# Kernel tuning notes

Measured on AMD Instinct MI355X. Metric: run time of the kernel, lower is better.

## Reference

```python
import jax, jax.numpy as jnp
import numpy as np

N_CAT, N_PER = 5, 20
N_NODES = N_CAT * N_PER  # 100
T, IN_DIM, H = 512, 256, 1024


def gru_seq(x, Wih, Whh, bih, bhh):
    # x: (B, T, IN). torch GRU (batch_first), returns all hidden states (B, T, H).
    B = x.shape[0]
    Hd = Whh.shape[1]
    xp = x @ Wih.T + bih  # (B, T, 3H) precomputed input projections

    def step(h, xt):
        gh = h @ Whh.T + bhh
        xr, xz, xn = jnp.split(xt, 3, axis=-1)
        hr, hz, hn = jnp.split(gh, 3, axis=-1)
        r = jax.nn.sigmoid(xr + hr)
        z = jax.nn.sigmoid(xz + hz)
        n = jnp.tanh(xn + r * hn)
        h_new = (1.0 - z) * n + z * h
        return h_new, h_new

    h0 = jnp.zeros((B, Hd), x.dtype)
    _, hs = jax.lax.scan(step, h0, jnp.swapaxes(xp, 0, 1))
    return jnp.swapaxes(hs, 0, 1)  # (B, T, H)


def attention_block(x, Wt, bt):
    # x: (B, T, D). Linear over the time axis, softmax over output-time axis.
    # w[b,u,d] = sum_t x[b,t,d] * Wt[u,t] + bt[u]
    w = jnp.einsum('btd,ut->bud', x, Wt) + bt[None, :, None]
    probs = jax.nn.softmax(w, axis=1)  # softmax over u (time) per (b, d)
    return jnp.sum(probs * x, axis=1)  # (B, D)


def gat_conv(x, edge_index, W, a_src, a_dst, bias):
    # Single-head PyG GATConv with default add_self_loops=True, neg slope 0.2.
    N = x.shape[0]
    loops = jnp.arange(N)
    src = jnp.concatenate([edge_index[0], loops])
    dst = jnp.concatenate([edge_index[1], loops])
    h = x @ W.T  # (N, D)
    alpha_s = h @ a_src  # (N,)
    alpha_d = h @ a_dst
    e = jax.nn.leaky_relu(alpha_s[src] + alpha_d[dst], negative_slope=0.2)
    # segment softmax over incoming edges per target node
    emax = jax.ops.segment_max(e, dst, num_segments=N)
    ex = jnp.exp(e - emax[dst])
    denom = jax.ops.segment_sum(ex, dst, num_segments=N)
    alpha = ex / denom[dst]
    out = jax.ops.segment_sum(alpha[:, None] * h[src], dst, num_segments=N)
    return out + bias


def setup_inputs() -> dict:
    key = jax.random.key(0)
    ks = jax.random.split(key, 24)
    s = 0.05

    def rn(k, shape):
        return jax.random.normal(k, shape, dtype=jnp.float32) * s

    # structured edge lists
    inner = []
    for c in range(N_CAT):
        for i in range(N_PER):
            for j in range(N_PER):
                if i != j:
                    inner.append((c * N_PER + i, c * N_PER + j))
    inner_edge = jnp.asarray(np.array(inner, dtype=np.int64).T)  # (2, 1900)
    outer = [(i, j) for i in range(N_CAT) for j in range(N_CAT) if i != j]
    outer_edge = jnp.asarray(np.array(outer, dtype=np.int64).T)  # (2, 20)

    return {
        'weekly_batch': jax.random.normal(ks[0], (N_NODES, T, IN_DIM), dtype=jnp.float32),
        'gru_Wih': rn(ks[1], (3 * H, IN_DIM)),
        'gru_Whh': rn(ks[2], (3 * H, H)),
        'gru_bih': rn(ks[3], (3 * H,)),
        'gru_bhh': rn(ks[4], (3 * H,)),
        'enc_att_W': rn(ks[5], (T, T)),
        'enc_att_b': rn(ks[6], (T,)),
        'pool_att_W': rn(ks[7], (N_PER, N_PER)),
        'pool_att_b': rn(ks[8], (N_PER,)),
        'inner_W': rn(ks[9], (H, H)),
        'inner_asrc': rn(ks[10], (H,)),
        'inner_adst': rn(ks[11], (H,)),
        'inner_b': rn(ks[12], (H,)),
        'cat_W': rn(ks[13], (H, H)),
        'cat_asrc': rn(ks[14], (H,)),
        'cat_adst': rn(ks[15], (H,)),
        'cat_b': rn(ks[16], (H,)),
        'fusion_W': rn(ks[17], (H, 3 * H)),
        'fusion_b': rn(ks[18], (H,)),
        'reg_W': rn(ks[19], (1, H)),
        'reg_b': rn(ks[20], (1,)),
        'cls_W': rn(ks[21], (1, H)),
        'cls_b': rn(ks[22], (1,)),
        'inner_edge': inner_edge,
        'outer_edge': outer_edge,
    }


def reference(weekly_batch, gru_Wih, gru_Whh, gru_bih, gru_bhh,
              enc_att_W, enc_att_b, pool_att_W, pool_att_b,
              inner_W, inner_asrc, inner_adst, inner_b,
              cat_W, cat_asrc, cat_adst, cat_b,
              fusion_W, fusion_b, reg_W, reg_b, cls_W, cls_b,
              inner_edge, outer_edge):
    # SequenceEncoder: GRU + (eval-mode dropout = identity) + attention pooling
    seq = gru_seq(weekly_batch.reshape(-1, T, IN_DIM), gru_Wih, gru_Whh, gru_bih, gru_bhh)
    v = attention_block(seq, enc_att_W, enc_att_b)  # (100, H)

    # inner GAT over all 100 nodes
    inner_emb = gat_conv(v, inner_edge, inner_W, inner_asrc, inner_adst, inner_b)
    inner_emb = inner_emb.reshape(N_CAT, N_PER, H)
    vv = v.reshape(N_CAT, N_PER, H)

    # pool 20 stocks -> 1 category vector, then category-level GAT
    cat_vec = attention_block(vv, pool_att_W, pool_att_b)  # (5, H)
    cat_vec = gat_conv(cat_vec, outer_edge, cat_W, cat_asrc, cat_adst, cat_b)
    cat_exp = jnp.broadcast_to(cat_vec[:, None, :], (N_CAT, N_PER, H))

    fusion = jnp.concatenate([vv, cat_exp, inner_emb], axis=-1)  # (5, 20, 3H)
    f = jax.nn.relu(fusion @ fusion_W.T + fusion_b)
    reg_out = (f @ reg_W.T + reg_b).reshape(-1)  # (100,)
    cls_out = jax.nn.sigmoid(f @ cls_W.T + cls_b).reshape(-1)  # (100,)
    return reg_out, cls_out
```

## Files before the change

### kernel.cpp

```cpp
#include <hip/hip_runtime.h>
#include <hip/hip_bf16.h>


typedef __bf16 bf16x8 __attribute__((ext_vector_type(8)));
typedef float  floatx4 __attribute__((ext_vector_type(4)));
typedef int    intx4  __attribute__((ext_vector_type(4)));

struct US8 { unsigned short u[8]; };

__device__ __forceinline__ unsigned short f2bf(float f) {
  unsigned u = __builtin_bit_cast(unsigned, f);
  u += 0x7fffu + ((u >> 16) & 1u);
  return (unsigned short)(u >> 16);
}
__device__ __forceinline__ float bf2f(unsigned short h) {
  return __builtin_bit_cast(float, ((unsigned)h) << 16);
}
__device__ __forceinline__ float sigm(float x) { return 1.f / (1.f + __expf(-x)); }

__device__ __forceinline__ void bar_lds() {
  asm volatile("s_waitcnt lgkmcnt(0)" ::: "memory");
  __builtin_amdgcn_s_barrier();
  asm volatile("" ::: "memory");
}

static const size_t OF_XBF   = 0;
static const size_t OF_HIST  = 26214400;
static const size_t OF_ENCW  = 131277824;
static const size_t OF_V     = 131802112;
static const size_t OF_HIN   = 132211712;
static const size_t OF_IEMB  = 132621312;
static const size_t OF_CATV  = 133030912;
static const size_t OF_CATH  = 133051392;
static const size_t OF_CATO  = 133071872;
static const size_t OF_FBUF  = 133092352;
static const size_t OF_FOUT  = 134321152;
static const size_t OF_FLAGS = 134730752;

__global__ void f2bf_kernel(const float* __restrict__ src, unsigned short* __restrict__ dst, int n4) {
  int i = blockIdx.x * 256 + threadIdx.x;
  if (i < n4) {
    float4 v = ((const float4*)src)[i];
    ushort4 o;
    o.x = f2bf(v.x); o.y = f2bf(v.y); o.z = f2bf(v.z); o.w = f2bf(v.w);
    ((ushort4*)dst)[i] = o;
  }
}

#define GRU_LDS 163136
__global__ void __launch_bounds__(320) gru_recur(
    const unsigned short* __restrict__ xbf,
    const float* __restrict__ Whh, const float* __restrict__ Wih,
    const float* __restrict__ bih, const float* __restrict__ bhh,
    unsigned short* hist, int* flags)
{
  extern __shared__ char smem[];
  unsigned* hbf  = (unsigned*)smem;
  unsigned short* Bw  = (unsigned short*)smem;
  float* biasl = (float*)(smem + 122880);
  float* ghp   = (float*)(smem + 123136);
  float* hfp   = (float*)(smem + 161536);

  const int tid  = threadIdx.x;
  const int lane = tid & 63;
  const int w    = tid >> 6;
  const int wg   = blockIdx.x;
  const int g    = wg >> 6;
  const int s    = wg & 63;
  const int gb   = g * 25;
  const int myq  = s >> 4;

  for (int o = tid; o < 7680; o += 320) {
    int kk, ln; const float* sp; unsigned short* dst;
    if (o < 5120) {
      int q = o >= 2560; int rem = o - q * 2560;
      kk = rem >> 6; ln = rem & 63;
      int l = ln & 15, ksub = ln >> 4, j = s * 16 + l;
      int k = kk * 32 + ksub * 8;
      sp = (k < 1024) ? (Whh + (size_t)(q * 1024 + j) * 1024 + k)
                      : (Wih + (size_t)(q * 1024 + j) * 256 + (k - 1024));
      dst = Bw + ((size_t)((q * 40 + kk) * 64 + ln)) * 8;
    } else if (o < 7168) {
      int o2 = o - 5120; kk = o2 >> 6; ln = o2 & 63;
      int l = ln & 15, ksub = ln >> 4, j = s * 16 + l;
      sp = Whh + (size_t)(2048 + j) * 1024 + kk * 32 + ksub * 8;
      dst = Bw + (size_t)(5120 + kk * 64 + ln) * 8;
    } else {
      int o3 = o - 7168; kk = o3 >> 6; ln = o3 & 63;
      int l = ln & 15, ksub = ln >> 4, j = s * 16 + l;
      sp = Wih + (size_t)(2048 + j) * 256 + kk * 32 + ksub * 8;
      dst = Bw + (size_t)(7168 + kk * 64 + ln) * 8;
    }
    float4 f0 = *(const float4*)sp;
    float4 f1 = *(const float4*)(sp + 4);
    dst[0] = f2bf(f0.x); dst[1] = f2bf(f0.y); dst[2] = f2bf(f0.z); dst[3] = f2bf(f0.w);
    dst[4] = f2bf(f1.x); dst[5] = f2bf(f1.y); dst[6] = f2bf(f1.z); dst[7] = f2bf(f1.w);
  }
  if (tid < 16) {
    int j = s * 16 + tid;
    biasl[tid]      = bih[j]        + bhh[j];
    biasl[16 + tid] = bih[1024 + j] + bhh[1024 + j];
    biasl[32 + tid] = bhh[2048 + j];
    biasl[48 + tid] = bih[2048 + j];
  }
  for (int i = tid; i < 400; i += 320) hfp[i] = 0.f;
  __syncthreads();

  bf16x8 Breg[24];
  #pragma unroll
  for (int lk = 0; lk < 8; lk++) {
    int kk = w * 8 + lk;
    Breg[lk * 3 + 0] = __builtin_bit_cast(bf16x8, *(const intx4*)(Bw + (size_t)((kk)      * 64 + lane) * 8));
    Breg[lk * 3 + 1] = __builtin_bit_cast(bf16x8, *(const intx4*)(Bw + (size_t)((40 + kk) * 64 + lane) * 8));
    const unsigned short* np = (w < 4)
        ? (Bw + (size_t)(5120 + kk * 64 + lane) * 8)
        : (Bw + (size_t)(7168 + (kk - 32) * 64 + lane) * 8);
    Breg[lk * 3 + 2] = __builtin_bit_cast(bf16x8, *(const intx4*)np);
  }

  const int kf_x = (lane >> 4) * 8;
  size_t baseA[2], rowx[2];
  #pragma unroll
  for (int mt = 0; mt < 2; mt++) {
    int m = mt * 16 + (lane & 15);
    int bb = (m < 25) ? m : 24;
    baseA[mt] = (size_t)((g * 64 + (lane >> 5)) * 400 + bb * 16 + ((lane >> 4) & 1) * 8);
    rowx[mt]  = (size_t)(gb + bb) * 512 * 256;
  }

  const int* pollline = flags + (wg * 4 + w) * 16;

  for (int t = 0; t < 512; t++) {
    if (w < 4) {
      for (;;) {
        int f = __hip_atomic_load(pollline + (lane & 15), __ATOMIC_RELAXED, __HIP_MEMORY_SCOPE_AGENT);
        if (__all(f >= t)) break;
      }
      asm volatile("" ::: "memory");
    }

    const unsigned short* hrow = hist + (size_t)t * 102400;
    floatx4 acc[2][3];
    #pragma unroll
    for (int mt = 0; mt < 2; mt++)
      #pragma unroll
      for (int gg = 0; gg < 3; gg++) acc[mt][gg] = floatx4{0.f, 0.f, 0.f, 0.f};

    #pragma unroll
    for (int lk = 0; lk < 8; lk++) {
      int kk = w * 8 + lk;
      #pragma unroll
      for (int mt = 0; mt < 2; mt++) {
        const unsigned short* ap = (w < 4)
            ? (hrow + baseA[mt] + (size_t)kk * 800)
            : (xbf + rowx[mt] + (size_t)t * 256 + (kk - 32) * 32 + kf_x);
        bf16x8 a = __builtin_bit_cast(bf16x8, *(const intx4*)ap);
        acc[mt][0] = __builtin_amdgcn_mfma_f32_16x16x32_bf16(a, Breg[lk * 3 + 0], acc[mt][0], 0, 0, 0);
        acc[mt][1] = __builtin_amdgcn_mfma_f32_16x16x32_bf16(a, Breg[lk * 3 + 1], acc[mt][1], 0, 0, 0);
        acc[mt][2] = __builtin_amdgcn_mfma_f32_16x16x32_bf16(a, Breg[lk * 3 + 2], acc[mt][2], 0, 0, 0);
      }
    }

    {
      int base = (lane & 15) * 20 + (lane >> 4) * 4;
      #pragma unroll
      for (int mt = 0; mt < 2; mt++)
        #pragma unroll
        for (int gg = 0; gg < 3; gg++)
          *(floatx4*)(ghp + (size_t)((w * 2 + mt) * 3 + gg) * 320 + base) = acc[mt][gg];
    }
    bar_lds();

    if (tid < 256) {
      int lp = tid >> 5, b = tid & 31;
      if (b < 25) {
        int mt2 = b >> 4, rr = b & 15;
        unsigned packed = 0;
        #pragma unroll
        for (int ii = 0; ii < 2; ii++) {
          int l = lp * 2 + ii;
          int off = l * 20 + rr;
          float ghr = 0.f, ghz = 0.f, ghnh = 0.f, ghnx;
          #pragma unroll
          for (int ww = 0; ww < 4; ww++) {
            const float* gq = ghp + (size_t)((ww * 2 + mt2) * 3) * 320 + off;
            ghr += gq[0]; ghz += gq[320]; ghnh += gq[640];
          }
          { const float* gq = ghp + (size_t)((4 * 2 + mt2) * 3) * 320 + off;
            ghr += gq[0]; ghz += gq[320]; ghnx = gq[640]; }
          float r = sigm(ghr + biasl[l]);
          float z = sigm(ghz + biasl[16 + l]);
          float nv = ghnx + biasl[48 + l] + r * (ghnh + biasl[32 + l]);
          nv = fminf(fmaxf(nv, -15.f), 15.f);
          float e2 = __expf(-2.f * nv);
          float n = (1.f - e2) / (1.f + e2);
          float ho = hfp[l * 25 + b];
          float hn = (1.f - z) * n + z * ho;
          hfp[l * 25 + b] = hn;
          packed |= ((unsigned)f2bf(hn)) << (16 * ii);
        }
        hbf[b * 8 + lp] = packed;
      }
    }
    bar_lds();

    if (w == 4) {
      if (lane < 50) {
        int b = lane >> 1, hs = lane & 1;
        intx4 d = *(const intx4*)&hbf[b * 8 + hs * 4];
        unsigned long long addr = (unsigned long long)(hist + (size_t)(t + 1) * 102400
                                  + (size_t)((g * 64 + s) * 400 + b * 16 + hs * 8));
        asm volatile("global_store_dwordx4 %0, %1, off sc0 sc1" :: "v"(addr), "v"(d) : "memory");
      }
      if (t < 511) {
        asm volatile("s_waitcnt vmcnt(0)" ::: "memory");
        __hip_atomic_store(flags + ((g * 64 + lane) * 4 + myq) * 16 + (s & 15), t + 1,
                           __ATOMIC_RELAXED, __HIP_MEMORY_SCOPE_AGENT);
      }
    }
  }
}

#define ATT_LDS 68096
__global__ void __launch_bounds__(512) att_pool(
    const unsigned short* __restrict__ hist,
    const unsigned short* __restrict__ encw,
    const float* __restrict__ encb,
    float* __restrict__ vout)
{
  extern __shared__ char smem[];
  unsigned short* Bs = (unsigned short*)smem;
  float* red  = (float*)(smem + 65536);
  float* cmax = (float*)(smem + 65536 + 2048);
  float* csum = (float*)(smem + 65536 + 2048 + 256);

  const int tid = threadIdx.x, w = tid >> 6, lane = tid & 63;
  const int q = lane >> 4, col = lane & 15;
  const int n0 = blockIdx.x * 64;
  const int bg = n0 >> 10, d0 = n0 & 1023;
  const int gA = bg / 25, rA = bg - gA * 25;

  for (int ii = 0; ii < 8; ii++) {
    int c = tid + 512 * ii;
    int t = c >> 3, dd = c & 7;
    int sA = (d0 >> 4) + (dd >> 1), hsA = dd & 1;
    intx4 li = *(const intx4*)(hist + (size_t)(t + 1) * 102400
                             + (size_t)((gA * 64 + sA) * 400 + rA * 16 + hsA * 8));
    US8 u8 = __builtin_bit_cast(US8, li);
    int kstep = t >> 5, ksub = (t >> 3) & 3, i = t & 7;
    int ntile = dd >> 1, nc0 = (dd & 1) * 8;
    unsigned short* dst = Bs + ((size_t)((kstep * 4 + ntile) * 64 + ksub * 16 + nc0)) * 8 + i;
    #pragma unroll
    for (int jj = 0; jj < 8; jj++) dst[jj * 8] = u8.u[jj];
  }
  __syncthreads();

  floatx4 acc[4][4];
  #pragma unroll
  for (int mi = 0; mi < 4; mi++)
    #pragma unroll
    for (int ni = 0; ni < 4; ni++) acc[mi][ni] = floatx4{0.f, 0.f, 0.f, 0.f};

  #pragma unroll 2
  for (int kk = 0; kk < 16; kk++) {
    int tch = kk * 32 + q * 8;
    bf16x8 af[4];
    #pragma unroll
    for (int mi = 0; mi < 4; mi++) {
      int u = (w * 4 + mi) * 16 + col;
      af[mi] = __builtin_bit_cast(bf16x8, *(const intx4*)(encw + (size_t)u * 512 + tch));
    }
    #pragma unroll
    for (int ni = 0; ni < 4; ni++) {
      bf16x8 bf = __builtin_bit_cast(bf16x8, *(const intx4*)(Bs + (size_t)((kk * 4 + ni) * 64 + lane) * 8));
      #pragma unroll
      for (int mi = 0; mi < 4; mi++)
        acc[mi][ni] = __builtin_amdgcn_mfma_f32_16x16x32_bf16(af[mi], bf, acc[mi][ni], 0, 0, 0);
    }
  }

  #pragma unroll
  for (int mi = 0; mi < 4; mi++) {
    int ub = (w * 4 + mi) * 16 + q * 4;
    float b0 = encb[ub], b1 = encb[ub + 1], b2 = encb[ub + 2], b3 = encb[ub + 3];
    #pragma unroll
    for (int ni = 0; ni < 4; ni++) {
      acc[mi][ni][0] += b0; acc[mi][ni][1] += b1; acc[mi][ni][2] += b2; acc[mi][ni][3] += b3;
    }
  }
  #pragma unroll
  for (int ni = 0; ni < 4; ni++) {
    float m = -1e30f;
    #pragma unroll
    for (int mi = 0; mi < 4; mi++)
      #pragma unroll
      for (int r = 0; r < 4; r++) m = fmaxf(m, acc[mi][ni][r]);
    m = fmaxf(m, __shfl_xor(m, 16)); m = fmaxf(m, __shfl_xor(m, 32));
    red[w * 64 + ni * 16 + col] = m;
  }
  __syncthreads();
  if (tid < 64) {
    float m = red[tid];
    for (int w2 = 1; w2 < 8; w2++) m = fmaxf(m, red[w2 * 64 + tid]);
    cmax[tid] = m;
  }
  __syncthreads();
  #pragma unroll
  for (int ni = 0; ni < 4; ni++) {
    float cm = cmax[ni * 16 + col];
    float sum = 0.f;
    #pragma unroll
    for (int mi = 0; mi < 4; mi++)
      #pragma unroll
      for (int r = 0; r < 4; r++) {
        float e = __expf(acc[mi][ni][r] - cm);
        acc[mi][ni][r] = e; sum += e;
      }
    sum += __shfl_xor(sum, 16); sum += __shfl_xor(sum, 32);
    red[w * 64 + ni * 16 + col] = sum;
  }
  __syncthreads();
  if (tid < 64) {
    float sm = 0.f;
    for (int w2 = 0; w2 < 8; w2++) sm += red[w2 * 64 + tid];
    csum[tid] = sm;
  }
  __syncthreads();
  #pragma unroll
  for (int ni = 0; ni < 4; ni++) {
    float p = 0.f;
    #pragma unroll
    for (int mi = 0; mi < 4; mi++) {
      int u0 = (w * 4 + mi) * 16 + q * 4;
      int ks = u0 >> 5, ksb = (u0 >> 3) & 3, i0 = u0 & 7;
      const unsigned short* hp = Bs + (size_t)((ks * 4 + ni) * 64 + ksb * 16 + col) * 8 + i0;
      p += acc[mi][ni][0] * bf2f(hp[0]) + acc[mi][ni][1] * bf2f(hp[1])
         + acc[mi][ni][2] * bf2f(hp[2]) + acc[mi][ni][3] * bf2f(hp[3]);
    }
    p += __shfl_xor(p, 16); p += __shfl_xor(p, 32);
    red[w * 64 + ni * 16 + col] = p;
  }
  __syncthreads();
  if (tid < 64) {
    float p = 0.f;
    for (int w2 = 0; w2 < 8; w2++) p += red[w2 * 64 + tid];
    vout[n0 + tid] = p / csum[tid];
  }
}

__global__ void gemm_bt(const float* __restrict__ A, const float* __restrict__ B,
                        float* __restrict__ C, int M, int N, int K,
                        const float* __restrict__ bias, int relu)
{
  __shared__ float Al[16][33];
  __shared__ float Bl[64][33];
  int tx = threadIdx.x;
  int nb = blockIdx.x, mb = blockIdx.y;
  int n = nb * 64 + (tx & 63);
  int mq = tx >> 6;
  float acc[4] = {0.f, 0.f, 0.f, 0.f};
  for (int k0 = 0; k0 < K; k0 += 32) {
    for (int e = tx; e < 512; e += 256) {
      int r = e >> 5, c = e & 31; int m = mb * 16 + r;
      Al[r][c] = (m < M) ? A[(size_t)m * K + k0 + c] : 0.f;
    }
    for (int e = tx; e < 2048; e += 256) {
      int r = e >> 5, c = e & 31;
      Bl[r][c] = B[(size_t)(nb * 64 + r) * K + k0 + c];
    }
    __syncthreads();
    int nn = tx & 63;
    #pragma unroll 8
    for (int c = 0; c < 32; c++) {
      float bv = Bl[nn][c];
      #pragma unroll
      for (int i = 0; i < 4; i++) acc[i] += Al[mq * 4 + i][c] * bv;
    }
    __syncthreads();
  }
  #pragma unroll
  for (int i = 0; i < 4; i++) {
    int m = mb * 16 + mq * 4 + i;
    if (m < M && n < N) {
      float r = acc[i] + (bias ? bias[n] : 0.f);
      if (relu) r = fmaxf(r, 0.f);
      C[(size_t)m * N + n] = r;
    }
  }
}

template <int NN>
__global__ void gat_att(const float* __restrict__ h, const float* __restrict__ asrc,
                        const float* __restrict__ adst, const float* __restrict__ bias,
                        float* __restrict__ out)
{
  __shared__ float asd[2][NN];
  __shared__ float P[NN][NN];
  int c = blockIdx.x, tx = threadIdx.x;
  int wid = tx >> 6, lane = tx & 63;
  for (int idx = wid; idx < 2 * NN; idx += 4) {
    int which = idx >= NN; int j = which ? idx - NN : idx;
    const float* av = which ? adst : asrc;
    float p = 0.f;
    for (int k = lane; k < 1024; k += 64) p += h[(size_t)(c * NN + j) * 1024 + k] * av[k];
    for (int m = 32; m; m >>= 1) p += __shfl_xor(p, m);
    if (lane == 0) asd[which][j] = p;
  }
  __syncthreads();
  if (tx < NN) {
    int i = tx; float mx = -1e30f; float e[NN];
    #pragma unroll
    for (int j = 0; j < NN; j++) {
      float x = asd[0][j] + asd[1][i];
      x = (x < 0.f) ? 0.2f * x : x;
      e[j] = x; mx = fmaxf(mx, x);
    }
    float s = 0.f;
    #pragma unroll
    for (int j = 0; j < NN; j++) { e[j] = __expf(e[j] - mx); s += e[j]; }
    #pragma unroll
    for (int j = 0; j < NN; j++) P[i][j] = e[j] / s;
  }
  __syncthreads();
  for (int ee = tx; ee < NN * 1024; ee += 256) {
    int i = ee >> 10, d = ee & 1023;
    float s = 0.f;
    #pragma unroll
    for (int j = 0; j < NN; j++) s += P[i][j] * h[(size_t)(c * NN + j) * 1024 + d];
    out[(size_t)(c * NN + i) * 1024 + d] = s + bias[d];
  }
}

__global__ void pool_att(const float* __restrict__ v, const float* __restrict__ pW,
                         const float* __restrict__ pb, float* __restrict__ catv)
{
  __shared__ float W[400]; __shared__ float bsh[20];
  int tx = threadIdx.x;
  for (int i = tx; i < 400; i += 256) W[i] = pW[i];
  if (tx < 20) bsh[tx] = pb[tx];
  __syncthreads();
  int gid = blockIdx.x * 256 + tx;
  int c = gid >> 10, d = gid & 1023;
  float vals[20];
  #pragma unroll
  for (int t = 0; t < 20; t++) vals[t] = v[(size_t)(c * 20 + t) * 1024 + d];
  float wv[20]; float mx = -1e30f;
  #pragma unroll
  for (int u = 0; u < 20; u++) {
    float s = bsh[u];
    #pragma unroll
    for (int t = 0; t < 20; t++) s += vals[t] * W[u * 20 + t];
    wv[u] = s; mx = fmaxf(mx, s);
  }
  float sum = 0.f, out = 0.f;
  #pragma unroll
  for (int u = 0; u < 20; u++) { float e = __expf(wv[u] - mx); sum += e; out += e * vals[u]; }
  catv[gid] = out / sum;
}

__global__ void concat_kernel(const float* __restrict__ v, const float* __restrict__ cato,
                              const float* __restrict__ iemb, float* __restrict__ F)
{
  int gid = blockIdx.x * 256 + threadIdx.x;
  if (gid < 307200) {
    int i = gid / 3072;
    int k = gid - i * 3072;
    float r;
    if (k < 1024)       r = v[(size_t)i * 1024 + k];
    else if (k < 2048)  r = cato[(size_t)(i / 20) * 1024 + (k - 1024)];
    else                r = iemb[(size_t)i * 1024 + (k - 2048)];
    F[gid] = r;
  }
}

__global__ void heads(const float* __restrict__ f, const float* __restrict__ rw,
                      const float* __restrict__ rb, const float* __restrict__ cw,
                      const float* __restrict__ cb, float* __restrict__ out)
{
  int b = blockIdx.x * 4 + (threadIdx.x >> 6);
  int lane = threadIdx.x & 63;
  float pr = 0.f, pc = 0.f;
  for (int k = lane; k < 1024; k += 64) {
    float x = f[(size_t)b * 1024 + k];
    pr += x * rw[k]; pc += x * cw[k];
  }
  for (int m = 32; m; m >>= 1) { pr += __shfl_xor(pr, m); pc += __shfl_xor(pc, m); }
  if (lane == 0) {
    out[b] = pr + rb[0];
    out[100 + b] = sigm(pc + cb[0]);
  }
}

extern "C" void kernel_launch(void* const* d_in, const int* in_sizes, int n_in,
                              void* d_out, int out_size, void* d_ws, size_t ws_size,
                              hipStream_t stream)
{
  const float* x     = (const float*)d_in[0];
  const float* Wih   = (const float*)d_in[1];
  const float* Whh   = (const float*)d_in[2];
  const float* bih   = (const float*)d_in[3];
  const float* bhh   = (const float*)d_in[4];
  const float* encW  = (const float*)d_in[5];
  const float* encb  = (const float*)d_in[6];
  const float* poolW = (const float*)d_in[7];
  const float* poolb = (const float*)d_in[8];
  const float* innW  = (const float*)d_in[9];
  const float* innas = (const float*)d_in[10];
  const float* innad = (const float*)d_in[11];
  const float* innb  = (const float*)d_in[12];
  const float* catW  = (const float*)d_in[13];
  const float* catas = (const float*)d_in[14];
  const float* catad = (const float*)d_in[15];
  const float* catb  = (const float*)d_in[16];
  const float* fusW  = (const float*)d_in[17];
  const float* fusb  = (const float*)d_in[18];
  const float* regW  = (const float*)d_in[19];
  const float* regb  = (const float*)d_in[20];
  const float* clsW  = (const float*)d_in[21];
  const float* clsb  = (const float*)d_in[22];
  float* out = (float*)d_out;
  char* ws = (char*)d_ws;

  unsigned short* xbf  = (unsigned short*)(ws + OF_XBF);
  unsigned short* hist = (unsigned short*)(ws + OF_HIST);
  int*            flg  = (int*)(ws + OF_FLAGS);
  unsigned short* ewbf = (unsigned short*)(ws + OF_ENCW);
  float* v    = (float*)(ws + OF_V);
  float* hin  = (float*)(ws + OF_HIN);
  float* iemb = (float*)(ws + OF_IEMB);
  float* catv = (float*)(ws + OF_CATV);
  float* cath = (float*)(ws + OF_CATH);
  float* cato = (float*)(ws + OF_CATO);
  float* fbuf = (float*)(ws + OF_FBUF);
  float* fout = (float*)(ws + OF_FOUT);

  (void)hipFuncSetAttribute((const void*)gru_recur, hipFuncAttributeMaxDynamicSharedMemorySize, GRU_LDS);
  (void)hipFuncSetAttribute((const void*)att_pool,  hipFuncAttributeMaxDynamicSharedMemorySize, ATT_LDS);

  (void)hipMemsetAsync(hist, 0, 204800, stream);
  (void)hipMemsetAsync(flg, 0, 65536, stream);

  f2bf_kernel<<<12800, 256, 0, stream>>>(x, xbf, 13107200 / 4);
  f2bf_kernel<<<256,   256, 0, stream>>>(encW, ewbf, 262144 / 4);

  gru_recur<<<256, 320, GRU_LDS, stream>>>(xbf, Whh, Wih, bih, bhh, hist, flg);
  att_pool<<<1600, 512, ATT_LDS, stream>>>(hist, ewbf, encb, v);

  gemm_bt<<<dim3(16, 7), 256, 0, stream>>>(v, innW, hin, 100, 1024, 1024, nullptr, 0);
  gat_att<20><<<5, 256, 0, stream>>>(hin, innas, innad, innb, iemb);
  pool_att<<<20, 256, 0, stream>>>(v, poolW, poolb, catv);
  gemm_bt<<<dim3(16, 1), 256, 0, stream>>>(catv, catW, cath, 5, 1024, 1024, nullptr, 0);
  gat_att<5><<<1, 256, 0, stream>>>(cath, catas, catad, catb, cato);
  concat_kernel<<<1200, 256, 0, stream>>>(v, cato, iemb, fbuf);
  gemm_bt<<<dim3(16, 7), 256, 0, stream>>>(fbuf, fusW, fout, 100, 1024, 3072, fusb, 1);
  heads<<<25, 256, 0, stream>>>(fout, regW, regb, clsW, clsb, out);

  (void)in_sizes; (void)n_in; (void)out_size; (void)ws_size;
}
```

Baseline: 4.219 ms.

## Streamline GRU step sync: direct per-wave stores, single flag writes, padded att LDS

In the persistent GRU recurrence, each of the four h-waves now runs the gate elementwise step for its own batch slice and stores bf16 hidden values straight to global memory. This drops the second LDS barrier and the staging through LDS by a separate wave. Flags change from being broadcast to all 64 consumers to one flag per producer wave, which consumers poll in a gathered pattern, so per-step flag traffic goes down. The att_pool kernel also pads its LDS B tile stride (514 shorts) and reorders the staging loop to reduce bank conflicts. The cost is narrower dword stores and 4x more flag reads per poll.

```diff
diff --git a/kernel.cpp b/kernel.cpp
--- a/kernel.cpp
+++ b/kernel.cpp
@@ -55,7 +55,6 @@
     unsigned short* hist, int* flags)
 {
   extern __shared__ char smem[];
-  unsigned* hbf  = (unsigned*)smem;
   unsigned short* Bw  = (unsigned short*)smem;
   float* biasl = (float*)(smem + 122880);
   float* ghp   = (float*)(smem + 123136);
@@ -68,7 +67,6 @@
   const int g    = wg >> 6;
   const int s    = wg & 63;
   const int gb   = g * 25;
-  const int myq  = s >> 4;
 
   for (int o = tid; o < 7680; o += 320) {
     int kk, ln; const float* sp; unsigned short* dst;
@@ -128,12 +126,14 @@
     rowx[mt]  = (size_t)(gb + bb) * 512 * 256;
   }
 
-  const int* pollline = flags + (wg * 4 + w) * 16;
+  const int* pollp = flags + (size_t)(g * 64 + w * 16 + ((lane >> 2) & 15)) * 16 + (lane & 3);
+  const int eb  = w * 8 + (lane >> 3);
+  const int elp = lane & 7;
 
   for (int t = 0; t < 512; t++) {
     if (w < 4) {
       for (;;) {
-        int f = __hip_atomic_load(pollline + (lane & 15), __ATOMIC_RELAXED, __HIP_MEMORY_SCOPE_AGENT);
+        int f = __hip_atomic_load(pollp, __ATOMIC_RELAXED, __HIP_MEMORY_SCOPE_AGENT);
         if (__all(f >= t)) break;
       }
       asm volatile("" ::: "memory");
@@ -171,14 +171,13 @@
     }
     bar_lds();
 
-    if (tid < 256) {
-      int lp = tid >> 5, b = tid & 31;
-      if (b < 25) {
-        int mt2 = b >> 4, rr = b & 15;
+    if (w < 4) {
+      if (eb < 25) {
+        int mt2 = eb >> 4, rr = eb & 15;
         unsigned packed = 0;
         #pragma unroll
         for (int ii = 0; ii < 2; ii++) {
-          int l = lp * 2 + ii;
+          int l = elp * 2 + ii;
           int off = l * 20 + rr;
           float ghr = 0.f, ghz = 0.f, ghnh = 0.f, ghnx;
           #pragma unroll
@@ -194,34 +193,26 @@
           nv = fminf(fmaxf(nv, -15.f), 15.f);
           float e2 = __expf(-2.f * nv);
           float n = (1.f - e2) / (1.f + e2);
-          float ho = hfp[l * 25 + b];
+          float ho = hfp[l * 25 + eb];
           float hn = (1.f - z) * n + z * ho;
-          hfp[l * 25 + b] = hn;
+          hfp[l * 25 + eb] = hn;
           packed |= ((unsigned)f2bf(hn)) << (16 * ii);
         }
-        hbf[b * 8 + lp] = packed;
-      }
-    }
-    bar_lds();
-
-    if (w == 4) {
-      if (lane < 50) {
-        int b = lane >> 1, hs = lane & 1;
-        intx4 d = *(const intx4*)&hbf[b * 8 + hs * 4];
         unsigned long long addr = (unsigned long long)(hist + (size_t)(t + 1) * 102400
-                                  + (size_t)((g * 64 + s) * 400 + b * 16 + hs * 8));
-        asm volatile("global_store_dwordx4 %0, %1, off sc0 sc1" :: "v"(addr), "v"(d) : "memory");
+                                  + (size_t)((g * 64 + s) * 400 + eb * 16 + elp * 2));
+        asm volatile("global_store_dword %0, %1, off sc0 sc1" :: "v"(addr), "v"(packed) : "memory");
       }
       if (t < 511) {
         asm volatile("s_waitcnt vmcnt(0)" ::: "memory");
-        __hip_atomic_store(flags + ((g * 64 + lane) * 4 + myq) * 16 + (s & 15), t + 1,
-                           __ATOMIC_RELAXED, __HIP_MEMORY_SCOPE_AGENT);
+        if (lane == 0)
+          __hip_atomic_store(flags + (size_t)wg * 16 + w, t + 1,
+                             __ATOMIC_RELAXED, __HIP_MEMORY_SCOPE_AGENT);
       }
     }
   }
 }
 
-#define ATT_LDS 68096
+#define ATT_LDS 68352
 __global__ void __launch_bounds__(512) att_pool(
     const unsigned short* __restrict__ hist,
     const unsigned short* __restrict__ encw,
@@ -230,9 +221,9 @@
 {
   extern __shared__ char smem[];
   unsigned short* Bs = (unsigned short*)smem;
-  float* red  = (float*)(smem + 65536);
-  float* cmax = (float*)(smem + 65536 + 2048);
-  float* csum = (float*)(smem + 65536 + 2048 + 256);
+  float* red  = (float*)(smem + 65792);
+  float* cmax = (float*)(smem + 65792 + 2048);
+  float* csum = (float*)(smem + 65792 + 2048 + 256);
 
   const int tid = threadIdx.x, w = tid >> 6, lane = tid & 63;
   const int q = lane >> 4, col = lane & 15;
@@ -242,14 +233,19 @@
 
   for (int ii = 0; ii < 8; ii++) {
     int c = tid + 512 * ii;
-    int t = c >> 3, dd = c & 7;
+    int dd   = c & 7;
+    int k8   = (c >> 3) & 7;
+    int i    = (c >> 6) & 7;
+    int ksub = (c >> 9) & 3;
+    int kshi = (c >> 11) & 1;
+    int kstep = kshi * 8 + k8;
+    int t = kstep * 32 + ksub * 8 + i;
     int sA = (d0 >> 4) + (dd >> 1), hsA = dd & 1;
     intx4 li = *(const intx4*)(hist + (size_t)(t + 1) * 102400
                              + (size_t)((gA * 64 + sA) * 400 + rA * 16 + hsA * 8));
     US8 u8 = __builtin_bit_cast(US8, li);
-    int kstep = t >> 5, ksub = (t >> 3) & 3, i = t & 7;
     int ntile = dd >> 1, nc0 = (dd & 1) * 8;
-    unsigned short* dst = Bs + ((size_t)((kstep * 4 + ntile) * 64 + ksub * 16 + nc0)) * 8 + i;
+    unsigned short* dst = Bs + (size_t)(kstep * 4 + ntile) * 514 + (ksub * 16 + nc0) * 8 + i;
     #pragma unroll
     for (int jj = 0; jj < 8; jj++) dst[jj * 8] = u8.u[jj];
   }
@@ -272,7 +268,7 @@
     }
     #pragma unroll
     for (int ni = 0; ni < 4; ni++) {
-      bf16x8 bf = __builtin_bit_cast(bf16x8, *(const intx4*)(Bs + (size_t)((kk * 4 + ni) * 64 + lane) * 8));
+      bf16x8 bf = __builtin_bit_cast(bf16x8, *(const intx4*)(Bs + (size_t)(kk * 4 + ni) * 514 + lane * 8));
       #pragma unroll
       for (int mi = 0; mi < 4; mi++)
         acc[mi][ni] = __builtin_amdgcn_mfma_f32_16x16x32_bf16(af[mi], bf, acc[mi][ni], 0, 0, 0);
@@ -333,7 +329,7 @@
     for (int mi = 0; mi < 4; mi++) {
       int u0 = (w * 4 + mi) * 16 + q * 4;
       int ks = u0 >> 5, ksb = (u0 >> 3) & 3, i0 = u0 & 7;
-      const unsigned short* hp = Bs + (size_t)((ks * 4 + ni) * 64 + ksb * 16 + col) * 8 + i0;
+      const unsigned short* hp = Bs + (size_t)(ks * 4 + ni) * 514 + (ksb * 16 + col) * 8 + i0;
       p += acc[mi][ni][0] * bf2f(hp[0]) + acc[mi][ni][1] * bf2f(hp[1])
          + acc[mi][ni][2] * bf2f(hp[2]) + acc[mi][ni][3] * bf2f(hp[3]);
     }
@@ -538,7 +534,7 @@
   (void)hipFuncSetAttribute((const void*)att_pool,  hipFuncAttributeMaxDynamicSharedMemorySize, ATT_LDS);
 
   (void)hipMemsetAsync(hist, 0, 204800, stream);
-  (void)hipMemsetAsync(flg, 0, 65536, stream);
+  (void)hipMemsetAsync(flg, 0, 16384, stream);
 
   f2bf_kernel<<<12800, 256, 0, stream>>>(x, xbf, 13107200 / 4);
   f2bf_kernel<<<256,   256, 0, stream>>>(encW, ewbf, 262144 / 4);
```

Result: slower. 4.504 ms (+6.7%).
